# Kernel tuning notes

Measured on AMD Instinct MI355X. Metric: run time of the kernel, lower is better.

Reference implementation:

```python
import jax, jax.numpy as jnp
import numpy as np


def setup_inputs() -> dict:
    key = jax.random.key(0)
    k1, k2, k3, k4 = jax.random.split(key, 4)
    B, S, T = 128, 512, 256
    return {
        "emissions": jax.random.normal(k1, (B, S, T), dtype=jnp.float32),
        "mask": jnp.ones((B, S), dtype=bool),
        "start_transitions": jax.random.normal(k2, (T,), dtype=jnp.float32),
        "end_transitions": jax.random.normal(k3, (T,), dtype=jnp.float32),
        "transitions": jax.random.normal(k4, (T, T), dtype=jnp.float32),
    }


def reference(emissions, mask, start_transitions, end_transitions, transitions):
    # emissions: [B, S, T], mask: [B, S] bool, transitions: [T, T]
    init = start_transitions[None, :] + emissions[:, 0]  # [B, T]
    em_t = jnp.swapaxes(emissions[:, 1:], 0, 1)  # [S-1, B, T] time-major
    mk_t = jnp.swapaxes(mask[:, 1:], 0, 1)       # [S-1, B]

    def lse_step(state, em):
        # state[b, i] + transitions[i, j] + em[b, j] -> logsumexp over i
        inner = state[:, :, None] + transitions[None, :, :] + em[:, None, :]
        return jax.nn.logsumexp(inner, axis=1)

    # _compute_score: mask-aware logsumexp recurrence (as written in the module)
    def step_score(score, xs):
        em, mk = xs
        nxt = lse_step(score, em)
        return jnp.where(mk[:, None], nxt, score), None

    score, _ = jax.lax.scan(step_score, init, (em_t, mk_t))
    score = jax.nn.logsumexp(score + end_transitions[None, :], axis=1)  # [B]

    # _compute_partition: same recurrence, mask where() is a no-op in the source
    def step_part(alpha, em):
        return lse_step(alpha, em), None

    alpha, _ = jax.lax.scan(step_part, init, em_t)
    partition = jax.nn.logsumexp(alpha + end_transitions[None, :], axis=1)  # [B]

    return partition - score
```

## Files before the change

### kernel.cpp

```cpp
#include <hip/hip_runtime.h>
#include <hip/hip_bf16.h>
#include <stdint.h>

#define LOG2E 1.44269504088896340736f
#define LN2   0.69314718055994530942f

typedef __attribute__((ext_vector_type(8))) __bf16 bf16x8;
typedef __attribute__((ext_vector_type(4))) float  f32x4;

static constexpr int B = 128, S = 512, T = 256;
static constexpr int LDP = T + 8;
static constexpr int H   = 260;
static constexpr int NSF = H;
static constexpr int NSB = S - 1 - H;

static __device__ __forceinline__ uint pack_bf16x2(float a, float b) {
    __hip_bfloat162 h = __float22bfloat162_rn(make_float2(a, b));
    union { __hip_bfloat162 h; uint u; } cv; cv.h = h;
    return cv.u;
}
static __device__ __forceinline__ float bf2f(ushort u) {
    return __uint_as_float(((uint)u) << 16);
}

static __device__ __forceinline__ void wg_barrier() {
    asm volatile("s_waitcnt lgkmcnt(0)" ::: "memory");
    __builtin_amdgcn_s_barrier();
    __builtin_amdgcn_sched_barrier(0);
}

static __device__ __forceinline__ float vmax24(const float v[2][4]) {
    float m = 0.0f;
    #pragma unroll
    for (int t = 0; t < 2; ++t)
        #pragma unroll
        for (int r = 0; r < 4; ++r) m = fmaxf(m, v[t][r]);
    return m;
}

__global__ void prep_mats(const float* __restrict__ trans,
                          ushort* __restrict__ Et, ushort* __restrict__ Em) {
    int i = blockIdx.x;
    int j = threadIdx.x;
    float e = exp2f(trans[i * T + j] * LOG2E);
    uint u = __float_as_uint(e);
    ushort h = (ushort)((u + 0x7FFFu + ((u >> 16) & 1u)) >> 16);
    Em[i * T + j] = h;
    Et[j * T + i] = h;
}

__global__ void prep_emx(const float* __restrict__ em, ushort* __restrict__ emx) {
    size_t i4 = ((size_t)blockIdx.x * blockDim.x + threadIdx.x) * 4;
    f32x4 e = *reinterpret_cast<const f32x4*>(&em[i4]);
    uint2 w;
    w.x = pack_bf16x2(exp2f(e[0] * LOG2E), exp2f(e[1] * LOG2E));
    w.y = pack_bf16x2(exp2f(e[2] * LOG2E), exp2f(e[3] * LOG2E));
    *reinterpret_cast<uint2*>(&emx[i4]) = w;
}

template<bool PRE, int DIR>
static __device__ __forceinline__ void scan_body(
    const float* __restrict__ em, const ushort* __restrict__ emx,
    const int* __restrict__ mask, const float* __restrict__ startt,
    const float* __restrict__ endt, const ushort* __restrict__ Amat,
    float* __restrict__ vecbuf, int* __restrict__ lsbuf,
    const int scan, const int bg,
    ushort (&Al)[2][16][LDP], float (&mx2)[16][8])
{
    constexpr int NSTEP = DIR ? NSB : NSF;
    constexpr int PGRP  = (NSTEP + 7) / 8;

    const int tid  = threadIdx.x;
    const int w    = tid >> 6;
    const int lane = tid & 63;
    const int q    = lane >> 4;
    const int l    = lane & 15;
    const int b    = bg * 16 + l;

    #define EROW(ix) (DIR ? (S - 2 - (ix)) : (1 + (ix)))
    #define MROW(ix) (DIR ? (S - 1 - (ix)) : (1 + (ix)))

    bf16x8 Afr[2][8];
    #pragma unroll
    for (int t = 0; t < 2; ++t) {
        int j = w * 32 + t * 16 + l;
        #pragma unroll
        for (int kt = 0; kt < 8; ++kt)
            Afr[t][kt] = *reinterpret_cast<const bf16x8*>(&Amat[j * T + kt * 32 + q * 8]);
    }

    const float*  emrow = em  + (size_t)b * S * T;
    const ushort* exrow = PRE ? emx + (size_t)b * S * T : nullptr;
    const int*    mrow  = mask + (size_t)b * S;

    int ls = 0;
    int buf = 0;
    float areg[2][4];

    {
        const int    r0 = DIR ? (S - 1) : 0;
        const float* tv = DIR ? endt : startt;
        float v0[2][4], gg[2][4]; float mx = 0.0f;
        #pragma unroll
        for (int t = 0; t < 2; ++t) {
            int j0 = w * 32 + t * 16 + q * 4;
            f32x4 e4 = *reinterpret_cast<const f32x4*>(&emrow[(size_t)r0 * T + j0]);
            f32x4 s4 = *reinterpret_cast<const f32x4*>(&tv[j0]);
            #pragma unroll
            for (int r = 0; r < 4; ++r) {
                float full = exp2f((e4[r] + s4[r]) * LOG2E);
                v0[t][r] = full;
                gg[t][r] = DIR ? exp2f(s4[r] * LOG2E) : full;
                mx = fmaxf(mx, full);
            }
        }
        mx = fmaxf(mx, __shfl_xor(mx, 16));
        mx = fmaxf(mx, __shfl_xor(mx, 32));
        if (q == 0) mx2[l][w] = mx;
        __syncthreads();
        f32x4 ma = *reinterpret_cast<const f32x4*>(&mx2[l][0]);
        f32x4 mb = *reinterpret_cast<const f32x4*>(&mx2[l][4]);
        float gmx = fmaxf(fmaxf(fmaxf(ma[0], ma[1]), fmaxf(ma[2], ma[3])),
                          fmaxf(fmaxf(mb[0], mb[1]), fmaxf(mb[2], mb[3])));
        int e = (int)((__float_as_uint(gmx) >> 23) & 255u) - 127;
        float sc = __uint_as_float((uint)(127 - e) << 23);
        ls = e;
        #pragma unroll
        for (int t = 0; t < 2; ++t) {
            int j0 = w * 32 + t * 16 + q * 4;
            uint2 wv;
            wv.x = pack_bf16x2(v0[t][0] * sc, v0[t][1] * sc);
            wv.y = pack_bf16x2(v0[t][2] * sc, v0[t][3] * sc);
            *reinterpret_cast<uint2*>(&Al[0][l][j0]) = wv;
            if (DIR) {
                #pragma unroll
                for (int r = 0; r < 4; ++r) areg[t][r] = gg[t][r] * sc;
            }
        }
        __syncthreads();
        if (q == 0) mx2[l][w] = mx * sc;
        __syncthreads();
    }

    const bool track = (DIR == 0) && (scan != 0);

    uint2 exv[8][2]; int mks[8];
    #pragma unroll
    for (int u = 0; u < 8; ++u) {
        int iu = u < NSTEP ? u : NSTEP - 1;
        #pragma unroll
        for (int t = 0; t < 2; ++t) {
            int j0 = w * 32 + t * 16 + q * 4;
            if (PRE) exv[u][t] = *reinterpret_cast<const uint2*>(&exrow[(size_t)EROW(iu) * T + j0]);
        }
        mks[u] = (scan && u < NSTEP) ? mrow[MROW(iu)] : 1;
    }

    for (int p = 0; p < PGRP; ++p) {
        uint2 exn[8][2]; int mkn[8];
        #pragma unroll
        for (int u = 0; u < 8; ++u) {
            int idx  = 8 * (p + 1) + u;
            int idxc = idx < NSTEP ? idx : NSTEP - 1;
            #pragma unroll
            for (int t = 0; t < 2; ++t) {
                int j0 = w * 32 + t * 16 + q * 4;
                if (PRE) exn[u][t] = *reinterpret_cast<const uint2*>(&exrow[(size_t)EROW(idxc) * T + j0]);
            }
            mkn[u] = (scan && idx < NSTEP) ? mrow[MROW(idxc)] : 1;
        }

        float pend = 1.0f, vml = 0.0f; int pk = 0;

        #pragma unroll
        for (int u = 0; u < 8; ++u) {
            const int idx = 8 * p + u;
            if (idx < NSTEP) {
                if ((u & 3) == 0) {
                    f32x4 ma = *reinterpret_cast<const f32x4*>(&mx2[l][0]);
                    f32x4 mb = *reinterpret_cast<const f32x4*>(&mx2[l][4]);
                    float gmx = fmaxf(fmaxf(fmaxf(ma[0], ma[1]), fmaxf(ma[2], ma[3])),
                                      fmaxf(fmaxf(mb[0], mb[1]), fmaxf(mb[2], mb[3])));
                    int kap = (int)((__float_as_uint(gmx) >> 23) & 255u) - 127;
                    pend = __uint_as_float((uint)(127 - kap) << 23);
                    pk   = kap;
                    vml  = gmx;
                }
                const int nb = buf ^ 1;

                bf16x8 bfr[8];
                #pragma unroll
                for (int kt = 0; kt < 8; ++kt)
                    bfr[kt] = *reinterpret_cast<const bf16x8*>(&Al[buf][l][kt * 32 + q * 8]);

                f32x4 ac[2][2] = {{f32x4{0,0,0,0}, f32x4{0,0,0,0}},
                                  {f32x4{0,0,0,0}, f32x4{0,0,0,0}}};
                #pragma unroll
                for (int kt = 0; kt < 8; ++kt) {
                    #pragma unroll
                    for (int t = 0; t < 2; ++t)
                        ac[t][kt & 1] = __builtin_amdgcn_mfma_f32_16x16x32_bf16(Afr[t][kt], bfr[kt], ac[t][kt & 1], 0, 0, 0);
                }
                f32x4 acc[2];
                #pragma unroll
                for (int t = 0; t < 2; ++t) acc[t] = ac[t][0] + ac[t][1];

                const int mk = mks[u];
                float v[2][4];

                #pragma unroll
                for (int t = 0; t < 2; ++t) {
                    float e_[4];
                    if (PRE) {
                        e_[0] = bf2f((ushort)(exv[u][t].x & 0xFFFF));
                        e_[1] = bf2f((ushort)(exv[u][t].x >> 16));
                        e_[2] = bf2f((ushort)(exv[u][t].y & 0xFFFF));
                        e_[3] = bf2f((ushort)(exv[u][t].y >> 16));
                    } else {
                        int j0 = w * 32 + t * 16 + q * 4;
                        f32x4 e4 = *reinterpret_cast<const f32x4*>(&emrow[(size_t)EROW(idx) * T + j0]);
                        #pragma unroll
                        for (int r = 0; r < 4; ++r) e_[r] = exp2f(e4[r] * LOG2E);
                    }
                    if (DIR == 0) {
                        #pragma unroll
                        for (int r = 0; r < 4; ++r)
                            v[t][r] = acc[t][r] * e_[r] * pend;
                    } else {
                        #pragma unroll
                        for (int r = 0; r < 4; ++r) {
                            float g  = acc[t][r] * pend;
                            float sv = mk ? g : areg[t][r];
                            areg[t][r] = sv;
                            v[t][r] = sv * e_[r];
                        }
                    }
                }

                if (DIR == 0) {
                    if (mk) {
                        #pragma unroll
                        for (int t = 0; t < 2; ++t) {
                            int j0 = w * 32 + t * 16 + q * 4;
                            uint2 wv;
                            wv.x = pack_bf16x2(v[t][0], v[t][1]);
                            wv.y = pack_bf16x2(v[t][2], v[t][3]);
                            *reinterpret_cast<uint2*>(&Al[nb][l][j0]) = wv;
                        }
                    } else {
                        #pragma unroll
                        for (int t = 0; t < 2; ++t) {
                            int j0 = w * 32 + t * 16 + q * 4;
                            *reinterpret_cast<uint2*>(&Al[nb][l][j0]) =
                                *reinterpret_cast<const uint2*>(&Al[buf][l][j0]);
                        }
                    }
                } else {
                    #pragma unroll
                    for (int t = 0; t < 2; ++t) {
                        int j0 = w * 32 + t * 16 + q * 4;
                        uint2 wv;
                        wv.x = pack_bf16x2(v[t][0], v[t][1]);
                        wv.y = pack_bf16x2(v[t][2], v[t][3]);
                        *reinterpret_cast<uint2*>(&Al[nb][l][j0]) = wv;
                    }
                }

                if (track) {
                    float lmx = vmax24(v);
                    vml = mk ? lmx : vml;
                }
                ls  += mk ? pk : 0;
                pend = mk ? 1.0f : pend;
                pk   = mk ? 0 : pk;

                const bool rn = ((u & 3) == 3) || (idx == NSTEP - 1);
                if (rn) {
                    float fm = track ? vml : vmax24(v);
                    fm = fmaxf(fm, __shfl_xor(fm, 16));
                    fm = fmaxf(fm, __shfl_xor(fm, 32));
                    if (q == 0) mx2[l][w] = fm;
                }

                wg_barrier();
                buf = nb;
            }
        }

        #pragma unroll
        for (int u = 0; u < 8; ++u) {
            #pragma unroll
            for (int t = 0; t < 2; ++t) exv[u][t] = exn[u][t];
            mks[u] = mkn[u];
        }
    }

    const int cidx = scan * 2 + DIR;
    if (DIR) {
        #pragma unroll
        for (int t = 0; t < 2; ++t) {
            int j0 = w * 32 + t * 16 + q * 4;
            f32x4 o = {areg[t][0], areg[t][1], areg[t][2], areg[t][3]};
            *reinterpret_cast<f32x4*>(&vecbuf[((size_t)cidx * B + b) * T + j0]) = o;
        }
    } else {
        #pragma unroll
        for (int t = 0; t < 2; ++t) {
            int j0 = w * 32 + t * 16 + q * 4;
            uint2 wv = *reinterpret_cast<const uint2*>(&Al[buf][l][j0]);
            f32x4 o = {bf2f((ushort)(wv.x & 0xFFFF)), bf2f((ushort)(wv.x >> 16)),
                       bf2f((ushort)(wv.y & 0xFFFF)), bf2f((ushort)(wv.y >> 16))};
            *reinterpret_cast<f32x4*>(&vecbuf[((size_t)cidx * B + b) * T + j0]) = o;
        }
    }
    if (w == 0 && q == 0) lsbuf[cidx * B + b] = ls;

    #undef EROW
    #undef MROW
}

template<bool PRE>
__launch_bounds__(512, 2)
__global__ void crf_scan(const float* __restrict__ em,
                         const ushort* __restrict__ emx,
                         const int* __restrict__ mask,
                         const float* __restrict__ startt,
                         const float* __restrict__ endt,
                         const ushort* __restrict__ Et,
                         const ushort* __restrict__ Emat,
                         float* __restrict__ vecbuf,
                         int* __restrict__ lsbuf)
{
    __shared__ __align__(16) ushort Al[2][16][LDP];
    __shared__ __align__(16) float mx2[16][8];

    const int scan = blockIdx.x & 1;
    const int dir  = (blockIdx.x >> 1) & 1;
    const int bg   = blockIdx.x >> 2;

    if (dir == 0)
        scan_body<PRE, 0>(em, emx, mask, startt, endt, Et,   vecbuf, lsbuf, scan, bg, Al, mx2);
    else
        scan_body<PRE, 1>(em, emx, mask, startt, endt, Emat, vecbuf, lsbuf, scan, bg, Al, mx2);
}

__global__ void combine2(const float* __restrict__ vecbuf, const int* __restrict__ lsbuf,
                         float* __restrict__ out) {
    __shared__ float r2[2][B];
    int tid = threadIdx.x;
    int sc_ = tid >> 7, b = tid & 127;
    const float* vf = vecbuf + ((size_t)(sc_ * 2 + 0) * B + b) * T;
    const float* vb = vecbuf + ((size_t)(sc_ * 2 + 1) * B + b) * T;
    float dot = 0.0f;
    for (int j = 0; j < T; j += 4) {
        f32x4 a = *reinterpret_cast<const f32x4*>(&vf[j]);
        f32x4 c = *reinterpret_cast<const f32x4*>(&vb[j]);
        dot += a[0] * c[0] + a[1] * c[1] + a[2] * c[2] + a[3] * c[3];
    }
    r2[sc_][b] = (float)(lsbuf[(sc_ * 2) * B + b] + lsbuf[(sc_ * 2 + 1) * B + b]) + log2f(dot);
    __syncthreads();
    if (tid < B) out[tid] = (r2[0][tid] - r2[1][tid]) * LN2;
}

extern "C" void kernel_launch(void* const* d_in, const int* in_sizes, int n_in,
                              void* d_out, int out_size, void* d_ws, size_t ws_size,
                              hipStream_t stream) {
    (void)in_sizes; (void)n_in; (void)out_size;
    const float* em = (const float*)d_in[0];
    const int*   mk = (const int*)d_in[1];
    const float* st = (const float*)d_in[2];
    const float* en = (const float*)d_in[3];
    const float* tr = (const float*)d_in[4];

    const size_t emx_bytes = (size_t)B * S * T * sizeof(ushort);
    const size_t mat_bytes = (size_t)T * T * sizeof(ushort);
    const size_t vec_bytes = (size_t)4 * B * T * sizeof(float);
    const size_t ls_bytes  = (size_t)4 * B * sizeof(int);

    const bool pre = ws_size >= emx_bytes + 2 * mat_bytes + vec_bytes + ls_bytes;

    char* wp = (char*)d_ws;
    ushort* emx = nullptr;
    if (pre) { emx = (ushort*)wp; wp += emx_bytes; }
    ushort* Et = (ushort*)wp; wp += mat_bytes;
    ushort* Em = (ushort*)wp; wp += mat_bytes;
    float*  vec = (float*)wp; wp += vec_bytes;
    int*    lsb = (int*)wp;

    prep_mats<<<T, T, 0, stream>>>(tr, Et, Em);
    if (pre) {
        prep_emx<<<(B * S * T) / (256 * 4), 256, 0, stream>>>(em, emx);
        crf_scan<true><<<32, 512, 0, stream>>>(em, emx, mk, st, en, Et, Em, vec, lsb);
    } else {
        crf_scan<false><<<32, 512, 0, stream>>>(em, emx, mk, st, en, Et, Em, vec, lsb);
    }
    combine2<<<1, 256, 0, stream>>>(vec, lsb, (float*)d_out);
}
```

Before: 383.4 us.

## Fuse score and partition scans into one block sharing emission loads

Each workgroup now runs both the mask-aware score recurrence and the unmasked partition recurrence for the same batch group and direction. They share the transition fragments held in registers, the emission loads and the per-step barrier. This halves the grid from 32 to 16 blocks and interleaves two independent MFMA chains per step. The aim is to remove duplicated global emission traffic and expose more instruction-level parallelism within the serial scan, at the cost of fewer active CUs, more registers and more LDS per block.

```diff
diff --git a/kernel.cpp b/kernel.cpp
--- a/kernel.cpp
+++ b/kernel.cpp
@@ -59,13 +59,12 @@
 }
 
 template<bool PRE, int DIR>
-static __device__ __forceinline__ void scan_body(
+static __device__ __forceinline__ void scan_pair_body(
     const float* __restrict__ em, const ushort* __restrict__ emx,
     const int* __restrict__ mask, const float* __restrict__ startt,
     const float* __restrict__ endt, const ushort* __restrict__ Amat,
-    float* __restrict__ vecbuf, int* __restrict__ lsbuf,
-    const int scan, const int bg,
-    ushort (&Al)[2][16][LDP], float (&mx2)[16][8])
+    float* __restrict__ vecbuf, int* __restrict__ lsbuf, const int bg,
+    ushort (&Al)[2][2][16][LDP], float (&mx2)[2][16][8])
 {
     constexpr int NSTEP = DIR ? NSB : NSF;
     constexpr int PGRP  = (NSTEP + 7) / 8;
@@ -93,9 +92,9 @@
     const ushort* exrow = PRE ? emx + (size_t)b * S * T : nullptr;
     const int*    mrow  = mask + (size_t)b * S;
 
-    int ls = 0;
+    int ls[2] = {0, 0};
     int buf = 0;
-    float areg[2][4];
+    float areg[2][2][4];
 
     {
         const int    r0 = DIR ? (S - 1) : 0;
@@ -116,33 +115,35 @@
         }
         mx = fmaxf(mx, __shfl_xor(mx, 16));
         mx = fmaxf(mx, __shfl_xor(mx, 32));
-        if (q == 0) mx2[l][w] = mx;
+        if (q == 0) { mx2[0][l][w] = mx; mx2[1][l][w] = mx; }
         __syncthreads();
-        f32x4 ma = *reinterpret_cast<const f32x4*>(&mx2[l][0]);
-        f32x4 mb = *reinterpret_cast<const f32x4*>(&mx2[l][4]);
+        f32x4 ma = *reinterpret_cast<const f32x4*>(&mx2[0][l][0]);
+        f32x4 mb = *reinterpret_cast<const f32x4*>(&mx2[0][l][4]);
         float gmx = fmaxf(fmaxf(fmaxf(ma[0], ma[1]), fmaxf(ma[2], ma[3])),
                           fmaxf(fmaxf(mb[0], mb[1]), fmaxf(mb[2], mb[3])));
         int e = (int)((__float_as_uint(gmx) >> 23) & 255u) - 127;
         float sc = __uint_as_float((uint)(127 - e) << 23);
-        ls = e;
+        ls[0] = e; ls[1] = e;
         #pragma unroll
         for (int t = 0; t < 2; ++t) {
             int j0 = w * 32 + t * 16 + q * 4;
             uint2 wv;
             wv.x = pack_bf16x2(v0[t][0] * sc, v0[t][1] * sc);
             wv.y = pack_bf16x2(v0[t][2] * sc, v0[t][3] * sc);
-            *reinterpret_cast<uint2*>(&Al[0][l][j0]) = wv;
+            *reinterpret_cast<uint2*>(&Al[0][0][l][j0]) = wv;
+            *reinterpret_cast<uint2*>(&Al[1][0][l][j0]) = wv;
             if (DIR) {
                 #pragma unroll
-                for (int r = 0; r < 4; ++r) areg[t][r] = gg[t][r] * sc;
+                for (int r = 0; r < 4; ++r) {
+                    areg[0][t][r] = gg[t][r] * sc;
+                    areg[1][t][r] = gg[t][r] * sc;
+                }
             }
         }
         __syncthreads();
-        if (q == 0) mx2[l][w] = mx * sc;
+        if (q == 0) { mx2[0][l][w] = mx * sc; mx2[1][l][w] = mx * sc; }
         __syncthreads();
     }
-
-    const bool track = (DIR == 0) && (scan != 0);
 
     uint2 exv[8][2]; int mks[8];
     #pragma unroll
@@ -153,7 +154,7 @@
             int j0 = w * 32 + t * 16 + q * 4;
             if (PRE) exv[u][t] = *reinterpret_cast<const uint2*>(&exrow[(size_t)EROW(iu) * T + j0]);
         }
-        mks[u] = (scan && u < NSTEP) ? mrow[MROW(iu)] : 1;
+        mks[u] = (u < NSTEP) ? mrow[MROW(iu)] : 1;
     }
 
     for (int p = 0; p < PGRP; ++p) {
@@ -167,92 +168,121 @@
                 int j0 = w * 32 + t * 16 + q * 4;
                 if (PRE) exn[u][t] = *reinterpret_cast<const uint2*>(&exrow[(size_t)EROW(idxc) * T + j0]);
             }
-            mkn[u] = (scan && idx < NSTEP) ? mrow[MROW(idxc)] : 1;
-        }
-
-        float pend = 1.0f, vml = 0.0f; int pk = 0;
+            mkn[u] = (idx < NSTEP) ? mrow[MROW(idxc)] : 1;
+        }
+
+        float pend[2] = {1.0f, 1.0f}, vml1 = 0.0f;
+        int pk[2] = {0, 0};
 
         #pragma unroll
         for (int u = 0; u < 8; ++u) {
             const int idx = 8 * p + u;
             if (idx < NSTEP) {
                 if ((u & 3) == 0) {
-                    f32x4 ma = *reinterpret_cast<const f32x4*>(&mx2[l][0]);
-                    f32x4 mb = *reinterpret_cast<const f32x4*>(&mx2[l][4]);
-                    float gmx = fmaxf(fmaxf(fmaxf(ma[0], ma[1]), fmaxf(ma[2], ma[3])),
-                                      fmaxf(fmaxf(mb[0], mb[1]), fmaxf(mb[2], mb[3])));
-                    int kap = (int)((__float_as_uint(gmx) >> 23) & 255u) - 127;
-                    pend = __uint_as_float((uint)(127 - kap) << 23);
-                    pk   = kap;
-                    vml  = gmx;
+                    #pragma unroll
+                    for (int c = 0; c < 2; ++c) {
+                        f32x4 ma = *reinterpret_cast<const f32x4*>(&mx2[c][l][0]);
+                        f32x4 mb = *reinterpret_cast<const f32x4*>(&mx2[c][l][4]);
+                        float gmx = fmaxf(fmaxf(fmaxf(ma[0], ma[1]), fmaxf(ma[2], ma[3])),
+                                          fmaxf(fmaxf(mb[0], mb[1]), fmaxf(mb[2], mb[3])));
+                        int kap = (int)((__float_as_uint(gmx) >> 23) & 255u) - 127;
+                        pend[c] = __uint_as_float((uint)(127 - kap) << 23);
+                        pk[c]   = kap;
+                        if (c == 1) vml1 = gmx;
+                    }
                 }
                 const int nb = buf ^ 1;
 
-                bf16x8 bfr[8];
-                #pragma unroll
-                for (int kt = 0; kt < 8; ++kt)
-                    bfr[kt] = *reinterpret_cast<const bf16x8*>(&Al[buf][l][kt * 32 + q * 8]);
-
-                f32x4 ac[2][2] = {{f32x4{0,0,0,0}, f32x4{0,0,0,0}},
-                                  {f32x4{0,0,0,0}, f32x4{0,0,0,0}}};
-                #pragma unroll
-                for (int kt = 0; kt < 8; ++kt) {
-                    #pragma unroll
-                    for (int t = 0; t < 2; ++t)
-                        ac[t][kt & 1] = __builtin_amdgcn_mfma_f32_16x16x32_bf16(Afr[t][kt], bfr[kt], ac[t][kt & 1], 0, 0, 0);
-                }
-                f32x4 acc[2];
-                #pragma unroll
-                for (int t = 0; t < 2; ++t) acc[t] = ac[t][0] + ac[t][1];
-
-                const int mk = mks[u];
-                float v[2][4];
-
+                f32x4 acc[2][2];
+                #pragma unroll
+                for (int c = 0; c < 2; ++c) {
+                    bf16x8 bfr[8];
+                    #pragma unroll
+                    for (int kt = 0; kt < 8; ++kt)
+                        bfr[kt] = *reinterpret_cast<const bf16x8*>(&Al[c][buf][l][kt * 32 + q * 8]);
+                    f32x4 ac[2][2] = {{f32x4{0,0,0,0}, f32x4{0,0,0,0}},
+                                      {f32x4{0,0,0,0}, f32x4{0,0,0,0}}};
+                    #pragma unroll
+                    for (int kt = 0; kt < 8; ++kt) {
+                        #pragma unroll
+                        for (int t = 0; t < 2; ++t)
+                            ac[t][kt & 1] = __builtin_amdgcn_mfma_f32_16x16x32_bf16(Afr[t][kt], bfr[kt], ac[t][kt & 1], 0, 0, 0);
+                    }
+                    acc[c][0] = ac[0][0] + ac[0][1];
+                    acc[c][1] = ac[1][0] + ac[1][1];
+                }
+
+                float e_[2][4];
                 #pragma unroll
                 for (int t = 0; t < 2; ++t) {
-                    float e_[4];
                     if (PRE) {
-                        e_[0] = bf2f((ushort)(exv[u][t].x & 0xFFFF));
-                        e_[1] = bf2f((ushort)(exv[u][t].x >> 16));
-                        e_[2] = bf2f((ushort)(exv[u][t].y & 0xFFFF));
-                        e_[3] = bf2f((ushort)(exv[u][t].y >> 16));
+                        e_[t][0] = bf2f((ushort)(exv[u][t].x & 0xFFFF));
+                        e_[t][1] = bf2f((ushort)(exv[u][t].x >> 16));
+                        e_[t][2] = bf2f((ushort)(exv[u][t].y & 0xFFFF));
+                        e_[t][3] = bf2f((ushort)(exv[u][t].y >> 16));
                     } else {
                         int j0 = w * 32 + t * 16 + q * 4;
                         f32x4 e4 = *reinterpret_cast<const f32x4*>(&emrow[(size_t)EROW(idx) * T + j0]);
                         #pragma unroll
-                        for (int r = 0; r < 4; ++r) e_[r] = exp2f(e4[r] * LOG2E);
-                    }
-                    if (DIR == 0) {
-                        #pragma unroll
-                        for (int r = 0; r < 4; ++r)
-                            v[t][r] = acc[t][r] * e_[r] * pend;
-                    } else {
-                        #pragma unroll
-                        for (int r = 0; r < 4; ++r) {
-                            float g  = acc[t][r] * pend;
-                            float sv = mk ? g : areg[t][r];
-                            areg[t][r] = sv;
-                            v[t][r] = sv * e_[r];
+                        for (int r = 0; r < 4; ++r) e_[t][r] = exp2f(e4[r] * LOG2E);
+                    }
+                }
+
+                const int mk1 = mks[u];
+                float v[2][2][4];
+
+                #pragma unroll
+                for (int t = 0; t < 2; ++t) {
+                    #pragma unroll
+                    for (int r = 0; r < 4; ++r) {
+                        if (DIR == 0) {
+                            v[0][t][r] = acc[0][t][r] * e_[t][r] * pend[0];
+                        } else {
+                            float g = acc[0][t][r] * pend[0];
+                            areg[0][t][r] = g;
+                            v[0][t][r] = g * e_[t][r];
                         }
                     }
                 }
-
+                #pragma unroll
+                for (int t = 0; t < 2; ++t) {
+                    #pragma unroll
+                    for (int r = 0; r < 4; ++r) {
+                        if (DIR == 0) {
+                            v[1][t][r] = acc[1][t][r] * e_[t][r] * pend[1];
+                        } else {
+                            float g  = acc[1][t][r] * pend[1];
+                            float sv = mk1 ? g : areg[1][t][r];
+                            areg[1][t][r] = sv;
+                            v[1][t][r] = sv * e_[t][r];
+                        }
+                    }
+                }
+
+                #pragma unroll
+                for (int t = 0; t < 2; ++t) {
+                    int j0 = w * 32 + t * 16 + q * 4;
+                    uint2 wv;
+                    wv.x = pack_bf16x2(v[0][t][0], v[0][t][1]);
+                    wv.y = pack_bf16x2(v[0][t][2], v[0][t][3]);
+                    *reinterpret_cast<uint2*>(&Al[0][nb][l][j0]) = wv;
+                }
                 if (DIR == 0) {
-                    if (mk) {
+                    if (mk1) {
                         #pragma unroll
                         for (int t = 0; t < 2; ++t) {
                             int j0 = w * 32 + t * 16 + q * 4;
                             uint2 wv;
-                            wv.x = pack_bf16x2(v[t][0], v[t][1]);
-                            wv.y = pack_bf16x2(v[t][2], v[t][3]);
-                            *reinterpret_cast<uint2*>(&Al[nb][l][j0]) = wv;
+                            wv.x = pack_bf16x2(v[1][t][0], v[1][t][1]);
+                            wv.y = pack_bf16x2(v[1][t][2], v[1][t][3]);
+                            *reinterpret_cast<uint2*>(&Al[1][nb][l][j0]) = wv;
                         }
                     } else {
                         #pragma unroll
                         for (int t = 0; t < 2; ++t) {
                             int j0 = w * 32 + t * 16 + q * 4;
-                            *reinterpret_cast<uint2*>(&Al[nb][l][j0]) =
-                                *reinterpret_cast<const uint2*>(&Al[buf][l][j0]);
+                            *reinterpret_cast<uint2*>(&Al[1][nb][l][j0]) =
+                                *reinterpret_cast<const uint2*>(&Al[1][buf][l][j0]);
                         }
                     }
                 } else {
@@ -260,26 +290,30 @@
                     for (int t = 0; t < 2; ++t) {
                         int j0 = w * 32 + t * 16 + q * 4;
                         uint2 wv;
-                        wv.x = pack_bf16x2(v[t][0], v[t][1]);
-                        wv.y = pack_bf16x2(v[t][2], v[t][3]);
-                        *reinterpret_cast<uint2*>(&Al[nb][l][j0]) = wv;
-                    }
-                }
-
-                if (track) {
-                    float lmx = vmax24(v);
-                    vml = mk ? lmx : vml;
-                }
-                ls  += mk ? pk : 0;
-                pend = mk ? 1.0f : pend;
-                pk   = mk ? 0 : pk;
+                        wv.x = pack_bf16x2(v[1][t][0], v[1][t][1]);
+                        wv.y = pack_bf16x2(v[1][t][2], v[1][t][3]);
+                        *reinterpret_cast<uint2*>(&Al[1][nb][l][j0]) = wv;
+                    }
+                }
+
+                ls[0] += pk[0]; pend[0] = 1.0f; pk[0] = 0;
+                ls[1] += mk1 ? pk[1] : 0;
+                pend[1] = mk1 ? 1.0f : pend[1];
+                pk[1]   = mk1 ? 0 : pk[1];
+                if (DIR == 0) {
+                    float lmx = vmax24(v[1]);
+                    vml1 = mk1 ? lmx : vml1;
+                }
 
                 const bool rn = ((u & 3) == 3) || (idx == NSTEP - 1);
                 if (rn) {
-                    float fm = track ? vml : vmax24(v);
-                    fm = fmaxf(fm, __shfl_xor(fm, 16));
-                    fm = fmaxf(fm, __shfl_xor(fm, 32));
-                    if (q == 0) mx2[l][w] = fm;
+                    float f0 = vmax24(v[0]);
+                    f0 = fmaxf(f0, __shfl_xor(f0, 16));
+                    f0 = fmaxf(f0, __shfl_xor(f0, 32));
+                    float f1 = (DIR == 0) ? vml1 : vmax24(v[1]);
+                    f1 = fmaxf(f1, __shfl_xor(f1, 16));
+                    f1 = fmaxf(f1, __shfl_xor(f1, 32));
+                    if (q == 0) { mx2[0][l][w] = f0; mx2[1][l][w] = f1; }
                 }
 
                 wg_barrier();
@@ -295,25 +329,28 @@
         }
     }
 
-    const int cidx = scan * 2 + DIR;
-    if (DIR) {
-        #pragma unroll
-        for (int t = 0; t < 2; ++t) {
-            int j0 = w * 32 + t * 16 + q * 4;
-            f32x4 o = {areg[t][0], areg[t][1], areg[t][2], areg[t][3]};
-            *reinterpret_cast<f32x4*>(&vecbuf[((size_t)cidx * B + b) * T + j0]) = o;
-        }
-    } else {
-        #pragma unroll
-        for (int t = 0; t < 2; ++t) {
-            int j0 = w * 32 + t * 16 + q * 4;
-            uint2 wv = *reinterpret_cast<const uint2*>(&Al[buf][l][j0]);
-            f32x4 o = {bf2f((ushort)(wv.x & 0xFFFF)), bf2f((ushort)(wv.x >> 16)),
-                       bf2f((ushort)(wv.y & 0xFFFF)), bf2f((ushort)(wv.y >> 16))};
-            *reinterpret_cast<f32x4*>(&vecbuf[((size_t)cidx * B + b) * T + j0]) = o;
-        }
-    }
-    if (w == 0 && q == 0) lsbuf[cidx * B + b] = ls;
+    #pragma unroll
+    for (int c = 0; c < 2; ++c) {
+        const int cidx = c * 2 + DIR;
+        if (DIR) {
+            #pragma unroll
+            for (int t = 0; t < 2; ++t) {
+                int j0 = w * 32 + t * 16 + q * 4;
+                f32x4 o = {areg[c][t][0], areg[c][t][1], areg[c][t][2], areg[c][t][3]};
+                *reinterpret_cast<f32x4*>(&vecbuf[((size_t)cidx * B + b) * T + j0]) = o;
+            }
+        } else {
+            #pragma unroll
+            for (int t = 0; t < 2; ++t) {
+                int j0 = w * 32 + t * 16 + q * 4;
+                uint2 wv = *reinterpret_cast<const uint2*>(&Al[c][buf][l][j0]);
+                f32x4 o = {bf2f((ushort)(wv.x & 0xFFFF)), bf2f((ushort)(wv.x >> 16)),
+                           bf2f((ushort)(wv.y & 0xFFFF)), bf2f((ushort)(wv.y >> 16))};
+                *reinterpret_cast<f32x4*>(&vecbuf[((size_t)cidx * B + b) * T + j0]) = o;
+            }
+        }
+        if (w == 0 && q == 0) lsbuf[cidx * B + b] = ls[c];
+    }
 
     #undef EROW
     #undef MROW
@@ -331,17 +368,16 @@
                          float* __restrict__ vecbuf,
                          int* __restrict__ lsbuf)
 {
-    __shared__ __align__(16) ushort Al[2][16][LDP];
-    __shared__ __align__(16) float mx2[16][8];
-
-    const int scan = blockIdx.x & 1;
-    const int dir  = (blockIdx.x >> 1) & 1;
-    const int bg   = blockIdx.x >> 2;
+    __shared__ __align__(16) ushort Al[2][2][16][LDP];
+    __shared__ __align__(16) float mx2[2][16][8];
+
+    const int dir = blockIdx.x & 1;
+    const int bg  = blockIdx.x >> 1;
 
     if (dir == 0)
-        scan_body<PRE, 0>(em, emx, mask, startt, endt, Et,   vecbuf, lsbuf, scan, bg, Al, mx2);
+        scan_pair_body<PRE, 0>(em, emx, mask, startt, endt, Et,   vecbuf, lsbuf, bg, Al, mx2);
     else
-        scan_body<PRE, 1>(em, emx, mask, startt, endt, Emat, vecbuf, lsbuf, scan, bg, Al, mx2);
+        scan_pair_body<PRE, 1>(em, emx, mask, startt, endt, Emat, vecbuf, lsbuf, bg, Al, mx2);
 }
 
 __global__ void combine2(const float* __restrict__ vecbuf, const int* __restrict__ lsbuf,
@@ -390,9 +426,9 @@
     prep_mats<<<T, T, 0, stream>>>(tr, Et, Em);
     if (pre) {
         prep_emx<<<(B * S * T) / (256 * 4), 256, 0, stream>>>(em, emx);
-        crf_scan<true><<<32, 512, 0, stream>>>(em, emx, mk, st, en, Et, Em, vec, lsb);
+        crf_scan<true><<<16, 512, 0, stream>>>(em, emx, mk, st, en, Et, Em, vec, lsb);
     } else {
-        crf_scan<false><<<32, 512, 0, stream>>>(em, emx, mk, st, en, Et, Em, vec, lsb);
+        crf_scan<false><<<16, 512, 0, stream>>>(em, emx, mk, st, en, Et, Em, vec, lsb);
     }
     combine2<<<1, 256, 0, stream>>>(vec, lsb, (float*)d_out);
 }
```

Measured after the change: 484.7 us. 26.4% more time.

## Fuse emission exponentiation into scan, drop prep kernel, parallelize combine

Applied to the files above, without the earlier changes.

Removes the separate prep_emx pass that converted all emissions to exponentiated bf16 in workspace. The scan now prefetches fp32 emissions four steps ahead (instead of eight bf16 steps) and computes exp2 inline. The forward/backward split point moves slightly, and the final combine runs one block per batch with shuffle reductions instead of a single serial block. This saves a full read and write pass over the emissions, but doubles the bytes the latency-bound scan loads per step and adds exp work inside the recurrence.

```diff
diff --git a/kernel.cpp b/kernel.cpp
--- a/kernel.cpp
+++ b/kernel.cpp
@@ -10,7 +10,7 @@
 
 static constexpr int B = 128, S = 512, T = 256;
 static constexpr int LDP = T + 8;
-static constexpr int H   = 260;
+static constexpr int H   = 258;
 static constexpr int NSF = H;
 static constexpr int NSB = S - 1 - H;
 
@@ -49,18 +49,9 @@
     Et[j * T + i] = h;
 }
 
-__global__ void prep_emx(const float* __restrict__ em, ushort* __restrict__ emx) {
-    size_t i4 = ((size_t)blockIdx.x * blockDim.x + threadIdx.x) * 4;
-    f32x4 e = *reinterpret_cast<const f32x4*>(&em[i4]);
-    uint2 w;
-    w.x = pack_bf16x2(exp2f(e[0] * LOG2E), exp2f(e[1] * LOG2E));
-    w.y = pack_bf16x2(exp2f(e[2] * LOG2E), exp2f(e[3] * LOG2E));
-    *reinterpret_cast<uint2*>(&emx[i4]) = w;
-}
-
-template<bool PRE, int DIR>
+template<int DIR>
 static __device__ __forceinline__ void scan_body(
-    const float* __restrict__ em, const ushort* __restrict__ emx,
+    const float* __restrict__ em,
     const int* __restrict__ mask, const float* __restrict__ startt,
     const float* __restrict__ endt, const ushort* __restrict__ Amat,
     float* __restrict__ vecbuf, int* __restrict__ lsbuf,
@@ -68,7 +59,7 @@
     ushort (&Al)[2][16][LDP], float (&mx2)[16][8])
 {
     constexpr int NSTEP = DIR ? NSB : NSF;
-    constexpr int PGRP  = (NSTEP + 7) / 8;
+    constexpr int PGRP  = (NSTEP + 3) / 4;
 
     const int tid  = threadIdx.x;
     const int w    = tid >> 6;
@@ -89,9 +80,8 @@
             Afr[t][kt] = *reinterpret_cast<const bf16x8*>(&Amat[j * T + kt * 32 + q * 8]);
     }
 
-    const float*  emrow = em  + (size_t)b * S * T;
-    const ushort* exrow = PRE ? emx + (size_t)b * S * T : nullptr;
-    const int*    mrow  = mask + (size_t)b * S;
+    const float* emrow = em  + (size_t)b * S * T;
+    const int*   mrow  = mask + (size_t)b * S;
 
     int ls = 0;
     int buf = 0;
@@ -144,28 +134,28 @@
 
     const bool track = (DIR == 0) && (scan != 0);
 
-    uint2 exv[8][2]; int mks[8];
+    f32x4 exv[4][2]; int mks[4];
     #pragma unroll
-    for (int u = 0; u < 8; ++u) {
+    for (int u = 0; u < 4; ++u) {
         int iu = u < NSTEP ? u : NSTEP - 1;
         #pragma unroll
         for (int t = 0; t < 2; ++t) {
             int j0 = w * 32 + t * 16 + q * 4;
-            if (PRE) exv[u][t] = *reinterpret_cast<const uint2*>(&exrow[(size_t)EROW(iu) * T + j0]);
+            exv[u][t] = *reinterpret_cast<const f32x4*>(&emrow[(size_t)EROW(iu) * T + j0]);
         }
         mks[u] = (scan && u < NSTEP) ? mrow[MROW(iu)] : 1;
     }
 
     for (int p = 0; p < PGRP; ++p) {
-        uint2 exn[8][2]; int mkn[8];
-        #pragma unroll
-        for (int u = 0; u < 8; ++u) {
-            int idx  = 8 * (p + 1) + u;
+        f32x4 exn[4][2]; int mkn[4];
+        #pragma unroll
+        for (int u = 0; u < 4; ++u) {
+            int idx  = 4 * (p + 1) + u;
             int idxc = idx < NSTEP ? idx : NSTEP - 1;
             #pragma unroll
             for (int t = 0; t < 2; ++t) {
                 int j0 = w * 32 + t * 16 + q * 4;
-                if (PRE) exn[u][t] = *reinterpret_cast<const uint2*>(&exrow[(size_t)EROW(idxc) * T + j0]);
+                exn[u][t] = *reinterpret_cast<const f32x4*>(&emrow[(size_t)EROW(idxc) * T + j0]);
             }
             mkn[u] = (scan && idx < NSTEP) ? mrow[MROW(idxc)] : 1;
         }
@@ -173,10 +163,10 @@
         float pend = 1.0f, vml = 0.0f; int pk = 0;
 
         #pragma unroll
-        for (int u = 0; u < 8; ++u) {
-            const int idx = 8 * p + u;
+        for (int u = 0; u < 4; ++u) {
+            const int idx = 4 * p + u;
             if (idx < NSTEP) {
-                if ((u & 3) == 0) {
+                if (u == 0) {
                     f32x4 ma = *reinterpret_cast<const f32x4*>(&mx2[l][0]);
                     f32x4 mb = *reinterpret_cast<const f32x4*>(&mx2[l][4]);
                     float gmx = fmaxf(fmaxf(fmaxf(ma[0], ma[1]), fmaxf(ma[2], ma[3])),
@@ -188,6 +178,13 @@
                 }
                 const int nb = buf ^ 1;
 
+                float ex_[2][4];
+                #pragma unroll
+                for (int t = 0; t < 2; ++t)
+                    #pragma unroll
+                    for (int r = 0; r < 4; ++r)
+                        ex_[t][r] = exp2f(exv[u][t][r] * LOG2E);
+
                 bf16x8 bfr[8];
                 #pragma unroll
                 for (int kt = 0; kt < 8; ++kt)
@@ -210,29 +207,17 @@
 
                 #pragma unroll
                 for (int t = 0; t < 2; ++t) {
-                    float e_[4];
-                    if (PRE) {
-                        e_[0] = bf2f((ushort)(exv[u][t].x & 0xFFFF));
-                        e_[1] = bf2f((ushort)(exv[u][t].x >> 16));
-                        e_[2] = bf2f((ushort)(exv[u][t].y & 0xFFFF));
-                        e_[3] = bf2f((ushort)(exv[u][t].y >> 16));
-                    } else {
-                        int j0 = w * 32 + t * 16 + q * 4;
-                        f32x4 e4 = *reinterpret_cast<const f32x4*>(&emrow[(size_t)EROW(idx) * T + j0]);
-                        #pragma unroll
-                        for (int r = 0; r < 4; ++r) e_[r] = exp2f(e4[r] * LOG2E);
-                    }
                     if (DIR == 0) {
                         #pragma unroll
                         for (int r = 0; r < 4; ++r)
-                            v[t][r] = acc[t][r] * e_[r] * pend;
+                            v[t][r] = acc[t][r] * ex_[t][r] * pend;
                     } else {
                         #pragma unroll
                         for (int r = 0; r < 4; ++r) {
                             float g  = acc[t][r] * pend;
                             float sv = mk ? g : areg[t][r];
                             areg[t][r] = sv;
-                            v[t][r] = sv * e_[r];
+                            v[t][r] = sv * ex_[t][r];
                         }
                     }
                 }
@@ -274,7 +259,7 @@
                 pend = mk ? 1.0f : pend;
                 pk   = mk ? 0 : pk;
 
-                const bool rn = ((u & 3) == 3) || (idx == NSTEP - 1);
+                const bool rn = (u == 3) || (idx == NSTEP - 1);
                 if (rn) {
                     float fm = track ? vml : vmax24(v);
                     fm = fmaxf(fm, __shfl_xor(fm, 16));
@@ -288,7 +273,7 @@
         }
 
         #pragma unroll
-        for (int u = 0; u < 8; ++u) {
+        for (int u = 0; u < 4; ++u) {
             #pragma unroll
             for (int t = 0; t < 2; ++t) exv[u][t] = exn[u][t];
             mks[u] = mkn[u];
@@ -319,10 +304,8 @@
     #undef MROW
 }
 
-template<bool PRE>
 __launch_bounds__(512, 2)
 __global__ void crf_scan(const float* __restrict__ em,
-                         const ushort* __restrict__ emx,
                          const int* __restrict__ mask,
                          const float* __restrict__ startt,
                          const float* __restrict__ endt,
@@ -339,60 +322,59 @@
     const int bg   = blockIdx.x >> 2;
 
     if (dir == 0)
-        scan_body<PRE, 0>(em, emx, mask, startt, endt, Et,   vecbuf, lsbuf, scan, bg, Al, mx2);
+        scan_body<0>(em, mask, startt, endt, Et,   vecbuf, lsbuf, scan, bg, Al, mx2);
     else
-        scan_body<PRE, 1>(em, emx, mask, startt, endt, Emat, vecbuf, lsbuf, scan, bg, Al, mx2);
+        scan_body<1>(em, mask, startt, endt, Emat, vecbuf, lsbuf, scan, bg, Al, mx2);
 }
 
 __global__ void combine2(const float* __restrict__ vecbuf, const int* __restrict__ lsbuf,
                          float* __restrict__ out) {
-    __shared__ float r2[2][B];
-    int tid = threadIdx.x;
-    int sc_ = tid >> 7, b = tid & 127;
-    const float* vf = vecbuf + ((size_t)(sc_ * 2 + 0) * B + b) * T;
-    const float* vb = vecbuf + ((size_t)(sc_ * 2 + 1) * B + b) * T;
-    float dot = 0.0f;
-    for (int j = 0; j < T; j += 4) {
-        f32x4 a = *reinterpret_cast<const f32x4*>(&vf[j]);
-        f32x4 c = *reinterpret_cast<const f32x4*>(&vb[j]);
-        dot += a[0] * c[0] + a[1] * c[1] + a[2] * c[2] + a[3] * c[3];
-    }
-    r2[sc_][b] = (float)(lsbuf[(sc_ * 2) * B + b] + lsbuf[(sc_ * 2 + 1) * B + b]) + log2f(dot);
+    const int b = blockIdx.x;
+    const int j = threadIdx.x;
+    const float* vf0 = vecbuf + ((size_t)0 * B + b) * T;
+    const float* vb0 = vecbuf + ((size_t)1 * B + b) * T;
+    const float* vf1 = vecbuf + ((size_t)2 * B + b) * T;
+    const float* vb1 = vecbuf + ((size_t)3 * B + b) * T;
+    float p0 = vf0[j] * vb0[j];
+    float p1 = vf1[j] * vb1[j];
+    #pragma unroll
+    for (int off = 32; off >= 1; off >>= 1) {
+        p0 += __shfl_xor(p0, off);
+        p1 += __shfl_xor(p1, off);
+    }
+    __shared__ float s0[4], s1[4];
+    const int wv = j >> 6, ln = j & 63;
+    if (ln == 0) { s0[wv] = p0; s1[wv] = p1; }
     __syncthreads();
-    if (tid < B) out[tid] = (r2[0][tid] - r2[1][tid]) * LN2;
+    if (j == 0) {
+        float d0 = (s0[0] + s0[1]) + (s0[2] + s0[3]);
+        float d1 = (s1[0] + s1[1]) + (s1[2] + s1[3]);
+        float r0 = (float)(lsbuf[0 * B + b] + lsbuf[1 * B + b]) + log2f(d0);
+        float r1 = (float)(lsbuf[2 * B + b] + lsbuf[3 * B + b]) + log2f(d1);
+        out[b] = (r0 - r1) * LN2;
+    }
 }
 
 extern "C" void kernel_launch(void* const* d_in, const int* in_sizes, int n_in,
                               void* d_out, int out_size, void* d_ws, size_t ws_size,
                               hipStream_t stream) {
-    (void)in_sizes; (void)n_in; (void)out_size;
+    (void)in_sizes; (void)n_in; (void)out_size; (void)ws_size;
     const float* em = (const float*)d_in[0];
     const int*   mk = (const int*)d_in[1];
     const float* st = (const float*)d_in[2];
     const float* en = (const float*)d_in[3];
     const float* tr = (const float*)d_in[4];
 
-    const size_t emx_bytes = (size_t)B * S * T * sizeof(ushort);
     const size_t mat_bytes = (size_t)T * T * sizeof(ushort);
     const size_t vec_bytes = (size_t)4 * B * T * sizeof(float);
-    const size_t ls_bytes  = (size_t)4 * B * sizeof(int);
-
-    const bool pre = ws_size >= emx_bytes + 2 * mat_bytes + vec_bytes + ls_bytes;
 
     char* wp = (char*)d_ws;
-    ushort* emx = nullptr;
-    if (pre) { emx = (ushort*)wp; wp += emx_bytes; }
     ushort* Et = (ushort*)wp; wp += mat_bytes;
     ushort* Em = (ushort*)wp; wp += mat_bytes;
     float*  vec = (float*)wp; wp += vec_bytes;
     int*    lsb = (int*)wp;
 
     prep_mats<<<T, T, 0, stream>>>(tr, Et, Em);
-    if (pre) {
-        prep_emx<<<(B * S * T) / (256 * 4), 256, 0, stream>>>(em, emx);
-        crf_scan<true><<<32, 512, 0, stream>>>(em, emx, mk, st, en, Et, Em, vec, lsb);
-    } else {
-        crf_scan<false><<<32, 512, 0, stream>>>(em, emx, mk, st, en, Et, Em, vec, lsb);
-    }
-    combine2<<<1, 256, 0, stream>>>(vec, lsb, (float*)d_out);
-}
+    crf_scan<<<32, 512, 0, stream>>>(em, mk, st, en, Et, Em, vec, lsb);
+    combine2<<<B, 256, 0, stream>>>(vec, lsb, (float*)d_out);
+}
```

New measurement: 345.8 us. 1.11x faster.
